# Kernel optimization log

Hardware: AMD Instinct MI355X
Metric: run time of the kernel (lower is better)

Reference implementation:

```python
import jax, jax.numpy as jnp
import numpy as np

K = 2           # top-k experts
TEMP = 1.0      # router temperature


def setup_inputs() -> dict:
    key = jax.random.key(0)
    k0, k1, k2, k3 = jax.random.split(key, 4)
    B, T, C, E = 4, 8192, 1024, 64
    x = jax.random.normal(k0, (B, T, C), dtype=jnp.float32)
    cond = jax.random.normal(k1, (B, C), dtype=jnp.float32)
    # nn.Linear weights: gate (E, C), cond_proj (C, 2C)
    Wg = jax.random.normal(k2, (E, C), dtype=jnp.float32) * 0.02
    Wc = jax.random.normal(k3, (C, 2 * C), dtype=jnp.float32) * 0.02
    return {"x": x, "cond": cond, "Wg": Wg, "Wc": Wc}


def reference(x, cond, Wg, Wc):
    B, T, C = x.shape
    E = Wg.shape[0]
    # conditioning path: broadcast cond over tokens, concat, project
    c_exp = jnp.broadcast_to(cond[:, None, :], (B, T, C))
    hc = jnp.concatenate([x, c_exp], axis=-1)          # (B,T,2C)
    h = jnp.einsum('btd,cd->btc', hc, Wc)              # (B,T,C)
    logits = jnp.einsum('btc,ec->bte', h, Wg) * (1.0 / TEMP)  # (B,T,E)
    probs = jax.nn.softmax(logits, axis=-1)
    topk_vals, idx = jax.lax.top_k(logits, K)          # (B,T,K), sorted desc
    scores = jax.nn.softmax(topk_vals, axis=-1)
    # aux stats (no_grad in torch)
    importance = jax.lax.stop_gradient(jnp.mean(probs, axis=(0, 1)))  # (E,)
    counts = jnp.zeros((E,), probs.dtype).at[idx.reshape(-1)].add(1.0)
    load = counts / jnp.clip(jnp.sum(counts), 1.0)
    load = jax.lax.stop_gradient(load)
    return (idx, scores, probs, importance, load)
```

## Files before the change

### kernel.cpp

```cpp
#include <hip/hip_runtime.h>
#include <math.h>

#define B_    4
#define T_    8192
#define C_    1024
#define E_    64
#define NTOK  (B_*T_)
#define KSEL  2

#define OFF_IDX    0
#define OFF_SCORES (NTOK*KSEL)
#define OFF_PROBS  (2*NTOK*KSEL)
#define OFF_IMP    (OFF_PROBS + NTOK*E_)
#define OFF_LOAD   (OFF_IMP + E_)

#define WS_W32    0
#define WS_BSWH   262144
#define WS_BSWL   393216
#define WS_LB64   524288
#define WS_CNT    526336
#define WS_LIST   526400

#define REFINE_CAP 8192
#define REFINE_EPS 3e-4f

typedef __attribute__((ext_vector_type(8))) short short8;
typedef __attribute__((ext_vector_type(4))) float f32x4;

__global__ __launch_bounds__(256) void k_prep(const float* __restrict__ Wg,
                                              const float* __restrict__ Wc,
                                              const float* __restrict__ cond,
                                              float* __restrict__ wcomb32,
                                              short* __restrict__ bswH,
                                              short* __restrict__ bswL,
                                              double* __restrict__ lbias64,
                                              float* __restrict__ out) {
    __shared__ float wg_s[64 * 64];
    __shared__ float wc_s[64 * 4];
    __shared__ double red[256];

    const int tid = threadIdx.x;
    const int e   = tid & 63;
    const int dg  = tid >> 6;
    const int d0  = blockIdx.x * 4;

    if (blockIdx.x == 0 && tid < 2 * E_) out[OFF_IMP + tid] = 0.f;

    double ae = 0.0, ao = 0.0;

    for (int c0 = 0; c0 < C_; c0 += 64) {
        __syncthreads();
#pragma unroll
        for (int k = 0; k < 4; ++k) {
            int li = tid + k * 256;
            int r = li >> 4, c4 = (li & 15) * 4;
            float4 v = *(const float4*)&Wg[(size_t)r * 1024 + c0 + c4];
            wg_s[(c4 + 0) * 64 + r] = v.x;
            wg_s[(c4 + 1) * 64 + r] = v.y;
            wg_s[(c4 + 2) * 64 + r] = v.z;
            wg_s[(c4 + 3) * 64 + r] = v.w;
        }
        if (tid < 128) {
            int cc = tid >> 1, dd0 = (tid & 1) * 2;
            *(float2*)&wc_s[cc * 4 + dd0] =
                *(const float2*)&Wc[(size_t)(c0 + cc) * 2048 + d0 + dd0];
        }
        __syncthreads();
#pragma unroll 8
        for (int c = 0; c < 64; c += 2) {
            ae += (double)wg_s[(c + 0) * 64 + e] * (double)wc_s[(c + 0) * 4 + dg];
            ao += (double)wg_s[(c + 1) * 64 + e] * (double)wc_s[(c + 1) * 4 + dg];
        }
    }
    const double acc = ae + ao;

    if (d0 < 1024) {
        const int d = d0 + dg;
        const int et = e >> 4, nn = e & 15;
        float f = (float)acc;
        wcomb32[d * 64 + e] = f;
        unsigned u = __float_as_uint(f);
        short hi = (short)(u >> 16);
        float r = f - __uint_as_float(u & 0xFFFF0000u);
        short lo = (short)(__float_as_uint(r) >> 16);
        int kchunk = d >> 5, qsel = (d >> 3) & 3, j = d & 7;
        int idx = ((kchunk * 4 + et) * 64 + qsel * 16 + nn) * 8 + j;
        bswH[idx] = hi;
        bswL[idx] = lo;
    } else {
        const int da = d0 - 1024 + dg;
#pragma unroll
        for (int b = 0; b < 4; ++b) {
            double pb = (double)cond[b * 1024 + da] * acc;
            __syncthreads();
            red[tid] = pb;
            __syncthreads();
            if (tid < 64) {
                double s = red[tid] + red[tid + 64] + red[tid + 128] + red[tid + 192];
#if __has_builtin(__builtin_amdgcn_global_atomic_fadd_f64)
                unsafeAtomicAdd(&lbias64[b * 64 + tid], s);
#else
                atomicAdd(&lbias64[b * 64 + tid], s);
#endif
            }
        }
    }
}

__device__ __forceinline__ void split8(const float* xv, short8& h, short8& l) {
#pragma unroll
    for (int j = 0; j < 8; ++j) {
        unsigned u = __float_as_uint(xv[j]);
        h[j] = (short)(u >> 16);
        float r = xv[j] - __uint_as_float(u & 0xFFFF0000u);
        l[j] = (short)(__float_as_uint(r) >> 16);
    }
}

#define MT    32
#define XSTR  132
#define BUFSZ (MT * XSTR)
#define ROWP  65

__global__ __launch_bounds__(256, 4) void k_main(const float* __restrict__ x,
                                                 const short* __restrict__ bswH,
                                                 const short* __restrict__ bswL,
                                                 const double* __restrict__ lbias64,
                                                 float* __restrict__ out,
                                                 unsigned int* __restrict__ ref_cnt,
                                                 int* __restrict__ ref_list) {
    __shared__ float xs[2 * BUFSZ];
    __shared__ float invs[MT];
    __shared__ unsigned int cnts[E_];

    const int tid    = threadIdx.x;
    const int wid    = tid >> 6;
    const int lane   = tid & 63;
    const int nn     = lane & 15;
    const int qsel   = lane >> 4;
    const int th     = wid & 1;
    const int eh     = wid >> 1;
    const int et0    = eh * 2;
    const int token0 = blockIdx.x * MT;
    const int b      = token0 >> 13;

    if (tid < E_) cnts[tid] = 0;

    f32x4 acc[2];
#pragma unroll
    for (int ei = 0; ei < 2; ++ei) acc[ei] = (f32x4){0.f, 0.f, 0.f, 0.f};

    const int srow = tid >> 5;
    const int scol = (tid & 31) * 4;

    f32x4 rg[4];
#pragma unroll
    for (int p = 0; p < 4; ++p)
        rg[p] = *(const f32x4*)&x[(size_t)(token0 + p * 8 + srow) * 1024 + scol];
#pragma unroll
    for (int p = 0; p < 4; ++p)
        *(f32x4*)&xs[(p * 8 + srow) * XSTR + scol] = rg[p];
    __syncthreads();

    const float* arow0 = &xs[(th * 16 + nn) * XSTR + qsel * 8];

    for (int t = 0; t < 8; ++t) {
        const int cur = t & 1;
        if (t < 7) {
            const int k0 = (t + 1) * 128;
#pragma unroll
            for (int p = 0; p < 4; ++p)
                rg[p] = *(const f32x4*)&x[(size_t)(token0 + p * 8 + srow) * 1024 + k0 + scol];
        }
        const float* arow = arow0 + cur * BUFSZ;
#pragma unroll
        for (int kc = 0; kc < 4; ++kc) {
            float xv[8];
            *(f32x4*)&xv[0] = *(const f32x4*)(arow + kc * 32);
            *(f32x4*)&xv[4] = *(const f32x4*)(arow + kc * 32 + 4);
            short8 ah, al;
            split8(xv, ah, al);
            const int kchunk = t * 4 + kc;
            const short* bh = bswH + (size_t)(kchunk * 4 + et0) * 512 + lane * 8;
            const short* bl = bswL + (size_t)(kchunk * 4 + et0) * 512 + lane * 8;
#pragma unroll
            for (int ei = 0; ei < 2; ++ei) {
                short8 b_h = *(const short8*)(bh + ei * 512);
                short8 b_l = *(const short8*)(bl + ei * 512);
                acc[ei] = __builtin_amdgcn_mfma_f32_16x16x32_bf16(ah, b_h, acc[ei], 0, 0, 0);
                acc[ei] = __builtin_amdgcn_mfma_f32_16x16x32_bf16(ah, b_l, acc[ei], 0, 0, 0);
                acc[ei] = __builtin_amdgcn_mfma_f32_16x16x32_bf16(al, b_h, acc[ei], 0, 0, 0);
            }
        }
        if (t < 7) {
#pragma unroll
            for (int p = 0; p < 4; ++p)
                *(f32x4*)&xs[(cur ^ 1) * BUFSZ + (p * 8 + srow) * XSTR + scol] = rg[p];
        }
        __syncthreads();
    }

    const int q4 = qsel * 4;
#pragma unroll
    for (int ei = 0; ei < 2; ++ei) {
        const int et = et0 + ei;
        float lb = (float)lbias64[b * 64 + et * 16 + nn];
#pragma unroll
        for (int r = 0; r < 4; ++r) {
            int tok = th * 16 + q4 + r;
            xs[tok * ROWP + et * 16 + nn] = acc[ei][r] + lb;
        }
    }
    __syncthreads();

    if (tid < MT) {
        const int tk = tid;
        const int base = tk * ROWP;
        float v1 = -1e30f, v2 = -1e30f, v3 = -1e30f;
        int i1 = 0, i2 = 0;
        for (int e = 0; e < E_; ++e) {
            float l = xs[base + e];
            if (l > v1)      { v3 = v2; v2 = v1; i2 = i1; v1 = l; i1 = e; }
            else if (l > v2) { v3 = v2; v2 = l; i2 = e; }
            else if (l > v3) { v3 = l; }
        }
        float sum = 0.f;
        for (int e = 0; e < E_; ++e) {
            float ex = __expf(xs[base + e] - v1);
            xs[base + e] = ex;
            sum += ex;
        }
        invs[tk] = 1.0f / sum;

        const int gt = token0 + tk;
        float s1 = 1.0f / (1.0f + __expf(v2 - v1));
        *(float2*)&out[OFF_IDX + (size_t)gt * 2]    = make_float2((float)i1, (float)i2);
        *(float2*)&out[OFF_SCORES + (size_t)gt * 2] = make_float2(s1, 1.0f - s1);
        atomicAdd(&cnts[i1], 1u);
        atomicAdd(&cnts[i2], 1u);

        float g12 = v1 - v2, g23 = v2 - v3;
        float g = g12 < g23 ? g12 : g23;
        if (g < REFINE_EPS) {
            unsigned int pos = atomicAdd(ref_cnt, 1u);
            if (pos < REFINE_CAP) ref_list[pos] = gt;
        }
    }
    __syncthreads();

    float* probs = out + OFF_PROBS + (size_t)token0 * E_;
#pragma unroll
    for (int k = 0; k < 2; ++k) {
        int li4 = tid + k * 256;
        int tok = li4 >> 4;
        int c4 = (li4 & 15) << 2;
        float inv = invs[tok];
        int o = tok * ROWP + c4;
        *(float4*)&probs[(size_t)li4 * 4] =
            make_float4(xs[o] * inv, xs[o + 1] * inv,
                        xs[o + 2] * inv, xs[o + 3] * inv);
    }

    if (tid < E_) {
        const int e = tid;
        float s = 0.f;
        for (int tt = 0; tt < MT; ++tt) s += xs[tt * ROWP + e] * invs[tt];
        atomicAdd(&out[OFF_IMP + e],  s * (1.0f / (float)NTOK));
        atomicAdd(&out[OFF_LOAD + e], (float)cnts[e] * (1.0f / (float)(NTOK * KSEL)));
    }
}

__global__ __launch_bounds__(256) void k_refine(const float* __restrict__ x,
                                                const float* __restrict__ wcomb32,
                                                const double* __restrict__ lbias64,
                                                const unsigned int* __restrict__ ref_cnt,
                                                const int* __restrict__ ref_list,
                                                float* __restrict__ out) {
    int wave = (int)((blockIdx.x * blockDim.x + threadIdx.x) >> 6);
    int lane = threadIdx.x & 63;
    unsigned int n = *ref_cnt;
    if (n > REFINE_CAP) n = REFINE_CAP;
    const int nwaves = (int)((gridDim.x * blockDim.x) >> 6);

    for (unsigned int wi = wave; wi < n; wi += nwaves) {
        const int gt = ref_list[wi];
        const int b = gt / T_;
        const float* xrow = x + (size_t)gt * C_;
        double a0 = 0.0, a1 = 0.0, a2 = 0.0, a3 = 0.0;
        for (int d = 0; d < C_; d += 4) {
            a0 += (double)xrow[d + 0] * (double)wcomb32[(d + 0) * 64 + lane];
            a1 += (double)xrow[d + 1] * (double)wcomb32[(d + 1) * 64 + lane];
            a2 += (double)xrow[d + 2] * (double)wcomb32[(d + 2) * 64 + lane];
            a3 += (double)xrow[d + 3] * (double)wcomb32[(d + 3) * 64 + lane];
        }
        double acc = ((a0 + a1) + (a2 + a3)) + lbias64[b * 64 + lane];

        double v = acc; int id = lane;
        for (int off = 32; off > 0; off >>= 1) {
            double ov = __shfl_xor(v, off, 64);
            int oid   = __shfl_xor(id, off, 64);
            if (ov > v || (ov == v && oid < id)) { v = ov; id = oid; }
        }
        double v1 = v; int i1 = id;
        v = (lane == i1) ? -1e300 : acc; id = lane;
        for (int off = 32; off > 0; off >>= 1) {
            double ov = __shfl_xor(v, off, 64);
            int oid   = __shfl_xor(id, off, 64);
            if (ov > v || (ov == v && oid < id)) { v = ov; id = oid; }
        }
        double v2 = v; int i2 = id;

        if (lane == 0) {
            float s1 = (float)(1.0 / (1.0 + exp(v2 - v1)));
            *(float2*)&out[OFF_IDX + (size_t)gt * 2]    = make_float2((float)i1, (float)i2);
            *(float2*)&out[OFF_SCORES + (size_t)gt * 2] = make_float2(s1, 1.0f - s1);
        }
    }
}

extern "C" void kernel_launch(void* const* d_in, const int* in_sizes, int n_in,
                              void* d_out, int out_size, void* d_ws, size_t ws_size,
                              hipStream_t stream) {
    const float* x    = (const float*)d_in[0];
    const float* cond = (const float*)d_in[1];
    const float* Wg   = (const float*)d_in[2];
    const float* Wc   = (const float*)d_in[3];
    float* out = (float*)d_out;
    char*  ws  = (char*)d_ws;

    float*  wcomb32 = (float*)(ws + WS_W32);
    short*  bswH    = (short*)(ws + WS_BSWH);
    short*  bswL    = (short*)(ws + WS_BSWL);
    double* lbias64 = (double*)(ws + WS_LB64);
    unsigned int* ref_cnt = (unsigned int*)(ws + WS_CNT);
    int*    ref_list = (int*)(ws + WS_LIST);

    hipMemsetAsync(ws + WS_LB64, 0, (WS_CNT - WS_LB64) + 64, stream);

    k_prep<<<512, 256, 0, stream>>>(Wg, Wc, cond, wcomb32, bswH, bswL, lbias64, out);
    k_main<<<NTOK / MT, 256, 0, stream>>>(x, bswH, bswL, lbias64, out, ref_cnt, ref_list);
    k_refine<<<256, 256, 0, stream>>>(x, wcomb32, lbias64, ref_cnt, ref_list, out);
}
```

Measured before the change: 342.2 us.

## Load x directly from global into MFMA registers, drop LDS double buffer

The main kernel no longer stages x tiles through a double-buffered shared-memory buffer with per-iteration barriers. Each lane now reads its A fragment straight from global memory, and all B fragments for a 128-wide K step are loaded into registers before the MFMAs. This removes the LDS round trip and the __syncthreads calls, shrinks LDS use, and may raise occupancy. In exchange, the global loads are strided per lane (32 bytes per row) and less coalesced, there is no explicit prefetch overlap, and register pressure rises.

```diff
diff --git a/kernel.cpp b/kernel.cpp
--- a/kernel.cpp
+++ b/kernel.cpp
@@ -118,8 +118,6 @@
 }
 
 #define MT    32
-#define XSTR  132
-#define BUFSZ (MT * XSTR)
 #define ROWP  65
 
 __global__ __launch_bounds__(256, 4) void k_main(const float* __restrict__ x,
@@ -129,7 +127,7 @@
                                                  float* __restrict__ out,
                                                  unsigned int* __restrict__ ref_cnt,
                                                  int* __restrict__ ref_list) {
-    __shared__ float xs[2 * BUFSZ];
+    __shared__ float ls[MT * ROWP];
     __shared__ float invs[MT];
     __shared__ unsigned int cnts[E_];
 
@@ -150,54 +148,36 @@
 #pragma unroll
     for (int ei = 0; ei < 2; ++ei) acc[ei] = (f32x4){0.f, 0.f, 0.f, 0.f};
 
-    const int srow = tid >> 5;
-    const int scol = (tid & 31) * 4;
-
-    f32x4 rg[4];
-#pragma unroll
-    for (int p = 0; p < 4; ++p)
-        rg[p] = *(const f32x4*)&x[(size_t)(token0 + p * 8 + srow) * 1024 + scol];
-#pragma unroll
-    for (int p = 0; p < 4; ++p)
-        *(f32x4*)&xs[(p * 8 + srow) * XSTR + scol] = rg[p];
-    __syncthreads();
-
-    const float* arow0 = &xs[(th * 16 + nn) * XSTR + qsel * 8];
+    const float* arow = &x[(size_t)(token0 + th * 16 + nn) * 1024 + qsel * 8];
+    const short* bh0  = bswH + (size_t)et0 * 512 + lane * 8;
+    const short* bl0  = bswL + (size_t)et0 * 512 + lane * 8;
 
     for (int t = 0; t < 8; ++t) {
-        const int cur = t & 1;
-        if (t < 7) {
-            const int k0 = (t + 1) * 128;
-#pragma unroll
-            for (int p = 0; p < 4; ++p)
-                rg[p] = *(const f32x4*)&x[(size_t)(token0 + p * 8 + srow) * 1024 + k0 + scol];
-        }
-        const float* arow = arow0 + cur * BUFSZ;
+        const int k0 = t * 128;
+        short8 Bh[4][2], Bl[4][2];
+#pragma unroll
+        for (int kc = 0; kc < 4; ++kc) {
+            const size_t soff = (size_t)((t * 4 + kc) * 4) * 512;
+#pragma unroll
+            for (int ei = 0; ei < 2; ++ei) {
+                Bh[kc][ei] = *(const short8*)(bh0 + soff + (size_t)ei * 512);
+                Bl[kc][ei] = *(const short8*)(bl0 + soff + (size_t)ei * 512);
+            }
+        }
 #pragma unroll
         for (int kc = 0; kc < 4; ++kc) {
             float xv[8];
-            *(f32x4*)&xv[0] = *(const f32x4*)(arow + kc * 32);
-            *(f32x4*)&xv[4] = *(const f32x4*)(arow + kc * 32 + 4);
+            *(f32x4*)&xv[0] = *(const f32x4*)(arow + k0 + kc * 32);
+            *(f32x4*)&xv[4] = *(const f32x4*)(arow + k0 + kc * 32 + 4);
             short8 ah, al;
             split8(xv, ah, al);
-            const int kchunk = t * 4 + kc;
-            const short* bh = bswH + (size_t)(kchunk * 4 + et0) * 512 + lane * 8;
-            const short* bl = bswL + (size_t)(kchunk * 4 + et0) * 512 + lane * 8;
 #pragma unroll
             for (int ei = 0; ei < 2; ++ei) {
-                short8 b_h = *(const short8*)(bh + ei * 512);
-                short8 b_l = *(const short8*)(bl + ei * 512);
-                acc[ei] = __builtin_amdgcn_mfma_f32_16x16x32_bf16(ah, b_h, acc[ei], 0, 0, 0);
-                acc[ei] = __builtin_amdgcn_mfma_f32_16x16x32_bf16(ah, b_l, acc[ei], 0, 0, 0);
-                acc[ei] = __builtin_amdgcn_mfma_f32_16x16x32_bf16(al, b_h, acc[ei], 0, 0, 0);
+                acc[ei] = __builtin_amdgcn_mfma_f32_16x16x32_bf16(ah, Bh[kc][ei], acc[ei], 0, 0, 0);
+                acc[ei] = __builtin_amdgcn_mfma_f32_16x16x32_bf16(ah, Bl[kc][ei], acc[ei], 0, 0, 0);
+                acc[ei] = __builtin_amdgcn_mfma_f32_16x16x32_bf16(al, Bh[kc][ei], acc[ei], 0, 0, 0);
             }
         }
-        if (t < 7) {
-#pragma unroll
-            for (int p = 0; p < 4; ++p)
-                *(f32x4*)&xs[(cur ^ 1) * BUFSZ + (p * 8 + srow) * XSTR + scol] = rg[p];
-        }
-        __syncthreads();
     }
 
     const int q4 = qsel * 4;
@@ -208,7 +188,7 @@
 #pragma unroll
         for (int r = 0; r < 4; ++r) {
             int tok = th * 16 + q4 + r;
-            xs[tok * ROWP + et * 16 + nn] = acc[ei][r] + lb;
+            ls[tok * ROWP + et * 16 + nn] = acc[ei][r] + lb;
         }
     }
     __syncthreads();
@@ -219,15 +199,15 @@
         float v1 = -1e30f, v2 = -1e30f, v3 = -1e30f;
         int i1 = 0, i2 = 0;
         for (int e = 0; e < E_; ++e) {
-            float l = xs[base + e];
+            float l = ls[base + e];
             if (l > v1)      { v3 = v2; v2 = v1; i2 = i1; v1 = l; i1 = e; }
             else if (l > v2) { v3 = v2; v2 = l; i2 = e; }
             else if (l > v3) { v3 = l; }
         }
         float sum = 0.f;
         for (int e = 0; e < E_; ++e) {
-            float ex = __expf(xs[base + e] - v1);
-            xs[base + e] = ex;
+            float ex = __expf(ls[base + e] - v1);
+            ls[base + e] = ex;
             sum += ex;
         }
         invs[tk] = 1.0f / sum;
@@ -257,14 +237,14 @@
         float inv = invs[tok];
         int o = tok * ROWP + c4;
         *(float4*)&probs[(size_t)li4 * 4] =
-            make_float4(xs[o] * inv, xs[o + 1] * inv,
-                        xs[o + 2] * inv, xs[o + 3] * inv);
+            make_float4(ls[o] * inv, ls[o + 1] * inv,
+                        ls[o + 2] * inv, ls[o + 3] * inv);
     }
 
     if (tid < E_) {
         const int e = tid;
         float s = 0.f;
-        for (int tt = 0; tt < MT; ++tt) s += xs[tt * ROWP + e] * invs[tt];
+        for (int tt = 0; tt < MT; ++tt) s += ls[tt * ROWP + e] * invs[tt];
         atomicAdd(&out[OFF_IMP + e],  s * (1.0f / (float)NTOK));
         atomicAdd(&out[OFF_LOAD + e], (float)cnts[e] * (1.0f / (float)(NTOK * KSEL)));
     }
```

Result: slower. 358.3 us (+4.7%).

## Stage x tiles via direct global-to-LDS loads with XOR swizzle

Applied to the files above, without the earlier changes.

Replaces the register-staged double-buffered copy of x into shared memory with global_load_lds direct transfers. The padded row stride is replaced by an XOR-swizzled layout so bank conflicts stay low without padding. Explicit vmcnt waits and raw barriers are used to sync. This removes the VGPR staging and the LDS write instructions, but relies on hand-written waitcnt accounting, which the compiler cannot check for correctness.

```diff
diff --git a/kernel.cpp b/kernel.cpp
--- a/kernel.cpp
+++ b/kernel.cpp
@@ -26,6 +26,10 @@
 
 typedef __attribute__((ext_vector_type(8))) short short8;
 typedef __attribute__((ext_vector_type(4))) float f32x4;
+
+#define BAR() do { asm volatile("" ::: "memory"); \
+                   __builtin_amdgcn_s_barrier();  \
+                   asm volatile("" ::: "memory"); } while (0)
 
 __global__ __launch_bounds__(256) void k_prep(const float* __restrict__ Wg,
                                               const float* __restrict__ Wc,
@@ -118,9 +122,24 @@
 }
 
 #define MT    32
-#define XSTR  132
-#define BUFSZ (MT * XSTR)
 #define ROWP  65
+
+__device__ __forceinline__ void stage_tile(const float* __restrict__ x,
+                                           float* xs, int token0, int t,
+                                           int buf, int wid, int lane) {
+#pragma unroll
+    for (int p = 0; p < 4; ++p) {
+        const int sbase = p * 256 + wid * 64;
+        const int s  = sbase + lane;
+        const int r  = s >> 5;
+        const int f  = (s & 31) ^ (r & 7);
+        const float* g = &x[(size_t)(token0 + r) * 1024 + t * 128 + f * 4];
+        float* l = xs + buf * 4096 + sbase * 4;
+        __builtin_amdgcn_global_load_lds(
+            (const __attribute__((address_space(1))) unsigned int*)g,
+            (__attribute__((address_space(3))) unsigned int*)l, 16, 0, 0);
+    }
+}
 
 __global__ __launch_bounds__(256, 4) void k_main(const float* __restrict__ x,
                                                  const short* __restrict__ bswH,
@@ -129,7 +148,7 @@
                                                  float* __restrict__ out,
                                                  unsigned int* __restrict__ ref_cnt,
                                                  int* __restrict__ ref_list) {
-    __shared__ float xs[2 * BUFSZ];
+    __shared__ __align__(16) float xs[2 * 4096];
     __shared__ float invs[MT];
     __shared__ unsigned int cnts[E_];
 
@@ -150,54 +169,41 @@
 #pragma unroll
     for (int ei = 0; ei < 2; ++ei) acc[ei] = (f32x4){0.f, 0.f, 0.f, 0.f};
 
-    const int srow = tid >> 5;
-    const int scol = (tid & 31) * 4;
-
-    f32x4 rg[4];
-#pragma unroll
-    for (int p = 0; p < 4; ++p)
-        rg[p] = *(const f32x4*)&x[(size_t)(token0 + p * 8 + srow) * 1024 + scol];
-#pragma unroll
-    for (int p = 0; p < 4; ++p)
-        *(f32x4*)&xs[(p * 8 + srow) * XSTR + scol] = rg[p];
-    __syncthreads();
-
-    const float* arow0 = &xs[(th * 16 + nn) * XSTR + qsel * 8];
+    const short* bh0 = bswH + (size_t)et0 * 512 + lane * 8;
+    const short* bl0 = bswL + (size_t)et0 * 512 + lane * 8;
+
+    const int rr = th * 16 + nn;
+    const int rx = rr & 7;
+
+    stage_tile(x, xs, token0, 0, 0, wid, lane);
 
     for (int t = 0; t < 8; ++t) {
         const int cur = t & 1;
-        if (t < 7) {
-            const int k0 = (t + 1) * 128;
-#pragma unroll
-            for (int p = 0; p < 4; ++p)
-                rg[p] = *(const f32x4*)&x[(size_t)(token0 + p * 8 + srow) * 1024 + k0 + scol];
-        }
-        const float* arow = arow0 + cur * BUFSZ;
+        if (t < 7) stage_tile(x, xs, token0, t + 1, cur ^ 1, wid, lane);
+        if (t < 7) asm volatile("s_waitcnt vmcnt(4)" ::: "memory");
+        else       asm volatile("s_waitcnt vmcnt(0)" ::: "memory");
+        BAR();
+
+        const float* abase = xs + cur * 4096 + rr * 128;
 #pragma unroll
         for (int kc = 0; kc < 4; ++kc) {
+            const int f0 = kc * 8 + qsel * 2;
             float xv[8];
-            *(f32x4*)&xv[0] = *(const f32x4*)(arow + kc * 32);
-            *(f32x4*)&xv[4] = *(const f32x4*)(arow + kc * 32 + 4);
+            *(f32x4*)&xv[0] = *(const f32x4*)(abase + (((f0    ) ^ rx) << 2));
+            *(f32x4*)&xv[4] = *(const f32x4*)(abase + (((f0 + 1) ^ rx) << 2));
             short8 ah, al;
             split8(xv, ah, al);
-            const int kchunk = t * 4 + kc;
-            const short* bh = bswH + (size_t)(kchunk * 4 + et0) * 512 + lane * 8;
-            const short* bl = bswL + (size_t)(kchunk * 4 + et0) * 512 + lane * 8;
+            const size_t soff = (size_t)((t * 4 + kc) * 4) * 512;
 #pragma unroll
             for (int ei = 0; ei < 2; ++ei) {
-                short8 b_h = *(const short8*)(bh + ei * 512);
-                short8 b_l = *(const short8*)(bl + ei * 512);
+                short8 b_h = *(const short8*)(bh0 + soff + (size_t)ei * 512);
+                short8 b_l = *(const short8*)(bl0 + soff + (size_t)ei * 512);
                 acc[ei] = __builtin_amdgcn_mfma_f32_16x16x32_bf16(ah, b_h, acc[ei], 0, 0, 0);
                 acc[ei] = __builtin_amdgcn_mfma_f32_16x16x32_bf16(ah, b_l, acc[ei], 0, 0, 0);
                 acc[ei] = __builtin_amdgcn_mfma_f32_16x16x32_bf16(al, b_h, acc[ei], 0, 0, 0);
             }
         }
-        if (t < 7) {
-#pragma unroll
-            for (int p = 0; p < 4; ++p)
-                *(f32x4*)&xs[(cur ^ 1) * BUFSZ + (p * 8 + srow) * XSTR + scol] = rg[p];
-        }
-        __syncthreads();
+        BAR();
     }
 
     const int q4 = qsel * 4;
```

Result: no change. 345.6 us (+1.0%).
